# Kernel optimization log

Measured on AMD Instinct MI355X. Metric: run time of the kernel, lower is better.

The kernel has to match this reference:

```python
import jax, jax.numpy as jnp
import numpy as np

E, CAP, D, F = 8, 4096, 1024, 4096  # experts, capacity/expert, d_model, d_ff


def setup_inputs() -> dict:
    key = jax.random.key(0)
    k0, k1, k2 = jax.random.split(key, 3)
    inputs = jax.random.normal(k0, (1, E * CAP, D), dtype=jnp.float32)
    # per-expert FFN params (stacked over expert axis)
    W1 = jax.random.normal(k1, (E, D, F), dtype=jnp.float32) * (1.0 / np.sqrt(D))
    b1 = jnp.zeros((E, F), dtype=jnp.float32)
    W2 = jax.random.normal(k2, (E, F, D), dtype=jnp.float32) * (1.0 / np.sqrt(F))
    b2 = jnp.zeros((E, D), dtype=jnp.float32)
    return {"inputs": inputs, "W1": W1, "b1": b1, "W2": W2, "b2": b2}


def reference(inputs, W1, b1, W2, b2):
    # inputs: [B, E*C, D]. chunk(dim=1) over E experts == reshape to [B, E, C, D].
    B, T, D_ = inputs.shape
    x = inputs.reshape(B, E, T // E, D_)  # [B, E, C, D]
    # grouped GEMM form of the per-expert loop: each expert applies its own FFN
    h = jax.nn.gelu(jnp.einsum('becd,edf->becf', x, W1) + b1[None, :, None, :])
    y = jnp.einsum('becf,efd->becd', h, W2) + b2[None, :, None, :]
    # cat over dim=1 == reshape back
    return y.reshape(B, T, D_)
```

## Files before the change

### kernel.cpp

```cpp
#include <hip/hip_runtime.h>
#include <stdint.h>

#define E_ 8
#define C_ 4096
#define D_ 1024
#define F_ 4096

typedef __attribute__((ext_vector_type(8))) short bf16x8;
typedef __attribute__((ext_vector_type(4))) float f32x4;
typedef __attribute__((ext_vector_type(8))) unsigned short u16x8;
typedef __attribute__((ext_vector_type(4))) unsigned short u16x4;

__device__ __forceinline__ unsigned short f2bf(float x) {
  union { float f; uint32_t u; } v; v.f = x;
  uint32_t r = v.u + 0x7FFFu + ((v.u >> 16) & 1u);
  return (unsigned short)(r >> 16);
}

__device__ __forceinline__ float gelu_f(float x) {
  float x3 = x * x * x;
  float u = 0.7978845608028654f * __builtin_fmaf(0.044715f, x3, x);
  float t = __expf(2.0f * u);
  float th = 1.0f - 2.0f / (t + 1.0f);
  return 0.5f * x * (1.0f + th);
}

__global__ void convert_bf16_kernel(const float* __restrict__ in,
                                    unsigned short* __restrict__ out, size_t n) {
  size_t i = ((size_t)blockIdx.x * blockDim.x + threadIdx.x) * 8;
  size_t stride = (size_t)gridDim.x * blockDim.x * 8;
  for (; i < n; i += stride) {
    float4 a = *(const float4*)(in + i);
    float4 b = *(const float4*)(in + i + 4);
    u16x8 o;
    o[0] = f2bf(a.x); o[1] = f2bf(a.y); o[2] = f2bf(a.z); o[3] = f2bf(a.w);
    o[4] = f2bf(b.x); o[5] = f2bf(b.y); o[6] = f2bf(b.z); o[7] = f2bf(b.w);
    *(u16x8*)(out + i) = o;
  }
}

__global__ void transpose_bf16_kernel(const float* __restrict__ in,
                                      unsigned short* __restrict__ out,
                                      int K, int N) {
  const int ge = blockIdx.z;
  const float* src = in + (size_t)ge * K * N;
  unsigned short* dst = out + (size_t)ge * K * N;
  __shared__ float tile[32][33];
  int t = threadIdx.x;
  int tx = t & 31, ty = t >> 5;
  int k0 = blockIdx.x * 32, n0 = blockIdx.y * 32;
#pragma unroll
  for (int p = 0; p < 4; ++p)
    tile[ty + p * 8][tx] = src[(size_t)(k0 + ty + p * 8) * N + n0 + tx];
  __syncthreads();
#pragma unroll
  for (int p = 0; p < 4; ++p)
    dst[(size_t)(n0 + ty + p * 8) * K + k0 + tx] = f2bf(tile[tx][ty + p * 8]);
}

typedef const __attribute__((address_space(1))) uint32_t* gas1_ptr;
typedef __attribute__((address_space(3))) uint32_t* las3_ptr;

__device__ __forceinline__ void async16(const void* g, void* l) {
  __builtin_amdgcn_global_load_lds((gas1_ptr)(uintptr_t)g, (las3_ptr)(uintptr_t)l,
                                   16, 0, 0);
}


#define SYNC_PRE() do { \
    __builtin_amdgcn_sched_barrier(0); \
    __builtin_amdgcn_s_barrier(); \
    asm volatile("s_waitcnt lgkmcnt(0)" ::: "memory"); \
    __builtin_amdgcn_sched_barrier(0); \
    __builtin_amdgcn_s_setprio(1); \
  } while (0)

#define SYNC_POST() do { \
    __builtin_amdgcn_s_setprio(0); \
    __builtin_amdgcn_sched_barrier(0); \
    __builtin_amdgcn_s_barrier(); \
    __builtin_amdgcn_sched_barrier(0); \
  } while (0)

#define SYNC_POST_VM() do { \
    __builtin_amdgcn_s_setprio(0); \
    __builtin_amdgcn_sched_barrier(0); \
    asm volatile("s_waitcnt vmcnt(6)" ::: "memory"); \
    __builtin_amdgcn_s_barrier(); \
    __builtin_amdgcn_sched_barrier(0); \
  } while (0)

template <int MODE>
__global__ __launch_bounds__(512, 2) void gemm256_kernel(
    const unsigned short* __restrict__ A,
    const unsigned short* __restrict__ B,
    const float* __restrict__ bias,
    void* __restrict__ Cout,
    int K, int N, int numM, int numN,
    size_t aStride, size_t bStride, size_t cStride, int biasStride) {
  __shared__ char lds[131072];
  char* ldsp = (char*)lds;

  const int NT = K >> 6;
  const int NITER = NT >> 1;

  int lin = blockIdx.x;
  int nwg = gridDim.x;
  int qq = nwg >> 3, rr8 = nwg & 7;
  int xcd = lin & 7, idx = lin >> 3;
  int wg = (xcd < rr8 ? xcd * (qq + 1) : rr8 * (qq + 1) + (xcd - rr8) * qq) + idx;
  int per = numM * numN;
  int e = wg / per;
  int rem = wg - e * per;
  int tm = rem % numM, tn = rem / numM;

  A += (size_t)e * aStride;
  B += (size_t)e * bStride;
  bias += (size_t)e * biasStride;

  const int rowTile = tm << 8;
  const int colTile = tn << 8;

  const int tid = threadIdx.x;
  const int lane = tid & 63;
  const int w = tid >> 6;
  const int wm = w & 1, wn = w >> 1;
  const int l15 = lane & 15, q = lane >> 4;

  const size_t ldB = (size_t)K * 2;

  const int rlo = tid >> 3, kc = tid & 7;
  const int swzsrc = ((kc ^ (rlo & 7)) << 4);
  const char* aS0 = (const char*)A + (size_t)(rowTile + rlo) * ldB + swzsrc;
  const char* aS1 = (const char*)A + (size_t)(rowTile + rlo + 128) * ldB + swzsrc;
  const int bcol = (rlo & 31) + ((rlo >> 5) << 6);
  const char* bS0 = (const char*)B + (size_t)(colTile + bcol) * ldB + swzsrc;
  const char* bS1 = (const char*)B + (size_t)(colTile + bcol + 128) * ldB + swzsrc;
  const size_t a64 = (size_t)64 * ldB;
  const size_t b32 = (size_t)32 * ldB;
  const int aD0 = rlo * 128 + kc * 16;
  const int aD1 = aD0 + 16384;
  const int bD0 = 32768 + bcol * 128 + kc * 16;
  const int bD1 = bD0 + 16384;

#define STAGE_A(bb, Ah, kt) do { \
    size_t kb = (size_t)(kt) * 128; \
    int dbase = (bb) * 65536 + (Ah) * 8192; \
    async16(aS0 + (Ah) * a64 + kb, ldsp + dbase + aD0); \
    async16(aS1 + (Ah) * a64 + kb, ldsp + dbase + aD1); \
  } while (0)

#define STAGE_B(bb, Bh, kt) do { \
    size_t kb = (size_t)(kt) * 128; \
    int dbase = (bb) * 65536 + (Bh) * 4096; \
    async16(bS0 + (Bh) * b32 + kb, ldsp + dbase + bD0); \
    async16(bS1 + (Bh) * b32 + kb, ldsp + dbase + bD1); \
  } while (0)

  const int k0 = (q * 16) ^ ((l15 & 7) << 4);
  const int aRdBase = wm * 16384 + l15 * 128;
  const int bRdBase = 32768 + wn * 8192 + l15 * 128;

  bf16x8 aR[4][2], bR0[2][2], bR1[2][2];
  f32x4 acc[8][4];
#pragma unroll
  for (int m = 0; m < 8; ++m)
#pragma unroll
    for (int n = 0; n < 4; ++n) acc[m][n] = {0.f, 0.f, 0.f, 0.f};

#define READ_A(bb, mh) do { \
    _Pragma("unroll") for (int m4 = 0; m4 < 4; ++m4) \
    _Pragma("unroll") for (int ks = 0; ks < 2; ++ks) \
      aR[m4][ks] = *(const bf16x8*)(ldsp + (bb) * 65536 + aRdBase + \
                                    ((mh) * 4 + m4) * 2048 + (k0 ^ (ks << 6))); \
  } while (0)

#define READ_B(dst, bb, nh) do { \
    _Pragma("unroll") for (int n2 = 0; n2 < 2; ++n2) \
    _Pragma("unroll") for (int ks = 0; ks < 2; ++ks) \
      dst[n2][ks] = *(const bf16x8*)(ldsp + (bb) * 65536 + bRdBase + \
                                     ((nh) * 2 + n2) * 2048 + (k0 ^ (ks << 6))); \
  } while (0)

#define MFMA_QUAD(mh, nh, BR) do { \
    _Pragma("unroll") for (int m4 = 0; m4 < 4; ++m4) \
    _Pragma("unroll") for (int n2 = 0; n2 < 2; ++n2) \
    _Pragma("unroll") for (int ks = 0; ks < 2; ++ks) \
      acc[(mh) * 4 + m4][(nh) * 2 + n2] = \
          __builtin_amdgcn_mfma_f32_16x16x32_bf16( \
              BR[n2][ks], aR[m4][ks], acc[(mh) * 4 + m4][(nh) * 2 + n2], 0, 0, 0); \
  } while (0)

  STAGE_A(0, 0, 0); STAGE_B(0, 0, 0); STAGE_A(0, 1, 0); STAGE_B(0, 1, 0);
  STAGE_A(1, 0, 1); STAGE_B(1, 0, 1); STAGE_A(1, 1, 1);
  asm volatile("s_waitcnt vmcnt(6)" ::: "memory");
  __builtin_amdgcn_sched_barrier(0);
  __builtin_amdgcn_s_barrier();
  __builtin_amdgcn_sched_barrier(0);

  for (int j = 0; j < NITER; ++j) {
    int t1 = 2 * j + 1;
    int t2 = 2 * j + 2; if (t2 > NT - 1) t2 = NT - 1;
    int t3 = 2 * j + 3; if (t3 > NT - 1) t3 = NT - 1;

    READ_A(0, 0); READ_B(bR0, 0, 0);
    STAGE_B(1, 1, t1);
    SYNC_PRE(); MFMA_QUAD(0, 0, bR0); SYNC_POST();
    READ_B(bR1, 0, 1);
    STAGE_A(0, 0, t2);
    SYNC_PRE(); MFMA_QUAD(0, 1, bR1); SYNC_POST();
    READ_A(0, 1);
    STAGE_B(0, 0, t2);
    SYNC_PRE(); MFMA_QUAD(1, 1, bR1); SYNC_POST();
    STAGE_A(0, 1, t2);
    SYNC_PRE(); MFMA_QUAD(1, 0, bR0); SYNC_POST_VM();
    READ_A(1, 0); READ_B(bR0, 1, 0);
    STAGE_B(0, 1, t2);
    SYNC_PRE(); MFMA_QUAD(0, 0, bR0); SYNC_POST();
    READ_B(bR1, 1, 1);
    STAGE_A(1, 0, t3);
    SYNC_PRE(); MFMA_QUAD(0, 1, bR1); SYNC_POST();
    READ_A(1, 1);
    STAGE_B(1, 0, t3);
    SYNC_PRE(); MFMA_QUAD(1, 1, bR1); SYNC_POST();
    STAGE_A(1, 1, t3);
    SYNC_PRE(); MFMA_QUAD(1, 0, bR0); SYNC_POST_VM();
  }
  asm volatile("s_waitcnt vmcnt(0)" ::: "memory");

#pragma unroll
  for (int mf = 0; mf < 8; ++mf) {
    int row = rowTile + wm * 128 + mf * 16 + l15;
#pragma unroll
    for (int nf = 0; nf < 4; ++nf) {
      int col = colTile + wn * 64 + nf * 16 + q * 4;
      float4 bv = *(const float4*)(bias + col);
      f32x4 v = acc[mf][nf];
      if constexpr (MODE == 1) {
        u16x4 o;
        o[0] = f2bf(gelu_f(v[0] + bv.x));
        o[1] = f2bf(gelu_f(v[1] + bv.y));
        o[2] = f2bf(gelu_f(v[2] + bv.z));
        o[3] = f2bf(gelu_f(v[3] + bv.w));
        *(u16x4*)((unsigned short*)Cout + (size_t)e * cStride +
                  (size_t)row * N + col) = o;
      } else {
        float4 o;
        o.x = v[0] + bv.x; o.y = v[1] + bv.y;
        o.z = v[2] + bv.z; o.w = v[3] + bv.w;
        *(float4*)((float*)Cout + (size_t)e * cStride + (size_t)row * N + col) = o;
      }
    }
  }
}

extern "C" void kernel_launch(void* const* d_in, const int* in_sizes, int n_in,
                              void* d_out, int out_size, void* d_ws, size_t ws_size,
                              hipStream_t stream) {
  const float* X = (const float*)d_in[0];
  const float* W1 = (const float*)d_in[1];
  const float* b1 = (const float*)d_in[2];
  const float* W2 = (const float*)d_in[3];
  const float* b2 = (const float*)d_in[4];
  float* Y = (float*)d_out;

  const size_t szX = (size_t)C_ * D_ * 2;
  const size_t szW1 = (size_t)F_ * D_ * 2;
  const size_t szW2 = (size_t)D_ * F_ * 2;
  const size_t szH = (size_t)C_ * F_ * 2;
  const size_t fixed = szX + szW1 + szW2;

  int g = 0;
  {
    const int cands[4] = {8, 4, 2, 1};
    for (int i = 0; i < 4; ++i)
      if ((fixed + szH) * (size_t)cands[i] <= ws_size) { g = cands[i]; break; }
  }
  int RC = C_;
  if (g == 0) {
    g = 1;
    size_t avail = ws_size > fixed ? ws_size - fixed : 0;
    RC = (int)(avail / ((size_t)F_ * 2));
    RC = (RC / 256) * 256;
    if (RC < 256) RC = 256;
    if (RC > C_) RC = C_;
  }

  unsigned short* XB = (unsigned short*)d_ws;
  unsigned short* W1T = XB + (size_t)g * C_ * D_;
  unsigned short* W2T = W1T + (size_t)g * F_ * D_;
  unsigned short* H = W2T + (size_t)g * D_ * F_;

  const int numN1 = F_ / 256;
  const int numN2 = D_ / 256;

  for (int e0 = 0; e0 < E_; e0 += g) {
    {
      size_t n = (size_t)g * C_ * D_;
      size_t nb = (n / 8 + 255) / 256;
      if (nb > 2048) nb = 2048;
      convert_bf16_kernel<<<dim3((unsigned)nb), 256, 0, stream>>>(
          X + (size_t)e0 * C_ * D_, XB, n);
    }
    transpose_bf16_kernel<<<dim3(D_ / 32, F_ / 32, g), 256, 0, stream>>>(
        W1 + (size_t)e0 * D_ * F_, W1T, D_, F_);
    transpose_bf16_kernel<<<dim3(F_ / 32, D_ / 32, g), 256, 0, stream>>>(
        W2 + (size_t)e0 * F_ * D_, W2T, F_, D_);

    for (int r0 = 0; r0 < C_; r0 += RC) {
      int numM = RC / 256;
      gemm256_kernel<1><<<dim3((unsigned)(numM * numN1 * g)), 512, 0, stream>>>(
          XB + (size_t)r0 * D_, W1T, b1 + (size_t)e0 * F_, (void*)H,
          D_, F_, numM, numN1,
          (size_t)C_ * D_, (size_t)F_ * D_, (size_t)RC * F_, F_);
      gemm256_kernel<0><<<dim3((unsigned)(numM * numN2 * g)), 512, 0, stream>>>(
          H, W2T, b2 + (size_t)e0 * D_,
          (void*)(Y + (size_t)e0 * C_ * D_ + (size_t)r0 * D_),
          F_, D_, numM, numN2,
          (size_t)RC * F_, (size_t)D_ * F_, (size_t)C_ * D_, D_);
    }
  }
}
```

Before: 725.2 us.

## Double-buffer LDS fragment registers and relax waitcnts in grouped GEMM main loop

Reworks the 256x256 bf16 MFMA main loop so A and B fragments are double-buffered in registers (even/odd sets), with next-phase LDS reads issued before the current MFMA quad. Waits are relaxed from full lgkmcnt(0) to partial vmcnt/lgkmcnt counts, letting LDS reads and global-to-LDS loads overlap with the MFMAs. Address arithmetic is simplified into precomputed int offsets, and the order of the prologue and in-loop staging is changed. This raises register pressure and relies on hand-tuned wait counts, which risk races if any count is wrong.

New measurement: 849.4 us. +17.1%, slower.

```diff
diff --git a/kernel.cpp b/kernel.cpp
--- a/kernel.cpp
+++ b/kernel.cpp
@@ -67,10 +67,10 @@
 }
 
 
-#define SYNC_PRE() do { \
+#define SYNC_PRE(VM, LG) do { \
     __builtin_amdgcn_sched_barrier(0); \
     __builtin_amdgcn_s_barrier(); \
-    asm volatile("s_waitcnt lgkmcnt(0)" ::: "memory"); \
+    asm volatile("s_waitcnt vmcnt(" #VM ") lgkmcnt(" #LG ")" ::: "memory"); \
     __builtin_amdgcn_sched_barrier(0); \
     __builtin_amdgcn_s_setprio(1); \
   } while (0)
@@ -78,14 +78,6 @@
 #define SYNC_POST() do { \
     __builtin_amdgcn_s_setprio(0); \
     __builtin_amdgcn_sched_barrier(0); \
-    __builtin_amdgcn_s_barrier(); \
-    __builtin_amdgcn_sched_barrier(0); \
-  } while (0)
-
-#define SYNC_POST_VM() do { \
-    __builtin_amdgcn_s_setprio(0); \
-    __builtin_amdgcn_sched_barrier(0); \
-    asm volatile("s_waitcnt vmcnt(6)" ::: "memory"); \
     __builtin_amdgcn_s_barrier(); \
     __builtin_amdgcn_sched_barrier(0); \
   } while (0)
@@ -131,102 +123,110 @@
 
   const int rlo = tid >> 3, kc = tid & 7;
   const int swzsrc = ((kc ^ (rlo & 7)) << 4);
-  const char* aS0 = (const char*)A + (size_t)(rowTile + rlo) * ldB + swzsrc;
-  const char* aS1 = (const char*)A + (size_t)(rowTile + rlo + 128) * ldB + swzsrc;
+  const int vA = (int)(rlo * (int)ldB) + swzsrc;
   const int bcol = (rlo & 31) + ((rlo >> 5) << 6);
-  const char* bS0 = (const char*)B + (size_t)(colTile + bcol) * ldB + swzsrc;
-  const char* bS1 = (const char*)B + (size_t)(colTile + bcol + 128) * ldB + swzsrc;
-  const size_t a64 = (size_t)64 * ldB;
-  const size_t b32 = (size_t)32 * ldB;
-  const int aD0 = rlo * 128 + kc * 16;
-  const int aD1 = aD0 + 16384;
-  const int bD0 = 32768 + bcol * 128 + kc * 16;
-  const int bD1 = bD0 + 16384;
+  const int vB = (int)(bcol * (int)ldB) + swzsrc;
+  const int dA = tid * 16;
+  const int dB = 32768 + (rlo & 31) * 128 + (rlo >> 5) * 8192 + kc * 16;
+  const char* Ag = (const char*)A + (size_t)rowTile * ldB;
+  const char* Bg = (const char*)B + (size_t)colTile * ldB;
+  const size_t r128 = (size_t)128 * ldB;
 
 #define STAGE_A(bb, Ah, kt) do { \
-    size_t kb = (size_t)(kt) * 128; \
-    int dbase = (bb) * 65536 + (Ah) * 8192; \
-    async16(aS0 + (Ah) * a64 + kb, ldsp + dbase + aD0); \
-    async16(aS1 + (Ah) * a64 + kb, ldsp + dbase + aD1); \
+    size_t u = (size_t)((Ah) * 64) * ldB + (size_t)(kt) * 128; \
+    async16(Ag + u + vA, ldsp + (bb) * 65536 + (Ah) * 8192 + dA); \
+    async16(Ag + u + r128 + vA, \
+            ldsp + (bb) * 65536 + (Ah) * 8192 + 16384 + dA); \
   } while (0)
 
 #define STAGE_B(bb, Bh, kt) do { \
-    size_t kb = (size_t)(kt) * 128; \
-    int dbase = (bb) * 65536 + (Bh) * 4096; \
-    async16(bS0 + (Bh) * b32 + kb, ldsp + dbase + bD0); \
-    async16(bS1 + (Bh) * b32 + kb, ldsp + dbase + bD1); \
+    size_t u = (size_t)((Bh) * 32) * ldB + (size_t)(kt) * 128; \
+    async16(Bg + u + vB, ldsp + (bb) * 65536 + (Bh) * 4096 + dB); \
+    async16(Bg + u + r128 + vB, \
+            ldsp + (bb) * 65536 + (Bh) * 4096 + 16384 + dB); \
   } while (0)
 
   const int k0 = (q * 16) ^ ((l15 & 7) << 4);
-  const int aRdBase = wm * 16384 + l15 * 128;
-  const int bRdBase = 32768 + wn * 8192 + l15 * 128;
-
-  bf16x8 aR[4][2], bR0[2][2], bR1[2][2];
+  const int iA00 = wm * 16384 + l15 * 128 + k0;
+  const int iA01 = iA00 ^ 64;
+  const int iA10 = iA00 + 65536;
+  const int iA11 = iA01 + 65536;
+  const int iB00 = 32768 + wn * 8192 + l15 * 128 + k0;
+  const int iB01 = iB00 ^ 64;
+  const int iB10 = iB00 + 65536;
+  const int iB11 = iB01 + 65536;
+
+  bf16x8 aE[4][2], aO[4][2], bZ[2][2], bY[2][2];
   f32x4 acc[8][4];
 #pragma unroll
   for (int m = 0; m < 8; ++m)
 #pragma unroll
     for (int n = 0; n < 4; ++n) acc[m][n] = {0.f, 0.f, 0.f, 0.f};
 
-#define READ_A(bb, mh) do { \
-    _Pragma("unroll") for (int m4 = 0; m4 < 4; ++m4) \
-    _Pragma("unroll") for (int ks = 0; ks < 2; ++ks) \
-      aR[m4][ks] = *(const bf16x8*)(ldsp + (bb) * 65536 + aRdBase + \
-                                    ((mh) * 4 + m4) * 2048 + (k0 ^ (ks << 6))); \
-  } while (0)
-
-#define READ_B(dst, bb, nh) do { \
-    _Pragma("unroll") for (int n2 = 0; n2 < 2; ++n2) \
-    _Pragma("unroll") for (int ks = 0; ks < 2; ++ks) \
-      dst[n2][ks] = *(const bf16x8*)(ldsp + (bb) * 65536 + bRdBase + \
-                                     ((nh) * 2 + n2) * 2048 + (k0 ^ (ks << 6))); \
-  } while (0)
-
-#define MFMA_QUAD(mh, nh, BR) do { \
+#define READ_A(dst, b0, b1, mh) do { \
+    _Pragma("unroll") for (int m4 = 0; m4 < 4; ++m4) { \
+      dst[m4][0] = *(const bf16x8*)(ldsp + (b0) + (mh) * 8192 + m4 * 2048); \
+      dst[m4][1] = *(const bf16x8*)(ldsp + (b1) + (mh) * 8192 + m4 * 2048); \
+    } \
+  } while (0)
+
+#define READ_B(dst, b0, b1, nh) do { \
+    _Pragma("unroll") for (int n2 = 0; n2 < 2; ++n2) { \
+      dst[n2][0] = *(const bf16x8*)(ldsp + (b0) + (nh) * 4096 + n2 * 2048); \
+      dst[n2][1] = *(const bf16x8*)(ldsp + (b1) + (nh) * 4096 + n2 * 2048); \
+    } \
+  } while (0)
+
+#define MFMA_Q(mh, nh, AF, BF) do { \
     _Pragma("unroll") for (int m4 = 0; m4 < 4; ++m4) \
     _Pragma("unroll") for (int n2 = 0; n2 < 2; ++n2) \
     _Pragma("unroll") for (int ks = 0; ks < 2; ++ks) \
       acc[(mh) * 4 + m4][(nh) * 2 + n2] = \
           __builtin_amdgcn_mfma_f32_16x16x32_bf16( \
-              BR[n2][ks], aR[m4][ks], acc[(mh) * 4 + m4][(nh) * 2 + n2], 0, 0, 0); \
-  } while (0)
-
-  STAGE_A(0, 0, 0); STAGE_B(0, 0, 0); STAGE_A(0, 1, 0); STAGE_B(0, 1, 0);
-  STAGE_A(1, 0, 1); STAGE_B(1, 0, 1); STAGE_A(1, 1, 1);
+              BF[n2][ks], AF[m4][ks], acc[(mh) * 4 + m4][(nh) * 2 + n2], 0, 0, 0); \
+  } while (0)
+
+  STAGE_A(0, 0, 0); STAGE_B(0, 0, 0); STAGE_B(0, 1, 0); STAGE_A(0, 1, 0);
+  STAGE_A(1, 0, 1); STAGE_B(1, 0, 1); STAGE_B(1, 1, 1);
   asm volatile("s_waitcnt vmcnt(6)" ::: "memory");
   __builtin_amdgcn_sched_barrier(0);
   __builtin_amdgcn_s_barrier();
   __builtin_amdgcn_sched_barrier(0);
+  READ_A(aE, iA00, iA01, 0);
+  READ_B(bZ, iB00, iB01, 0);
 
   for (int j = 0; j < NITER; ++j) {
     int t1 = 2 * j + 1;
     int t2 = 2 * j + 2; if (t2 > NT - 1) t2 = NT - 1;
     int t3 = 2 * j + 3; if (t3 > NT - 1) t3 = NT - 1;
 
-    READ_A(0, 0); READ_B(bR0, 0, 0);
-    STAGE_B(1, 1, t1);
-    SYNC_PRE(); MFMA_QUAD(0, 0, bR0); SYNC_POST();
-    READ_B(bR1, 0, 1);
+    READ_B(bY, iB00, iB01, 1);
+    STAGE_A(1, 1, t1);
+    SYNC_PRE(8, 4); MFMA_Q(0, 0, aE, bZ); SYNC_POST();
+    READ_A(aO, iA00, iA01, 1);
     STAGE_A(0, 0, t2);
-    SYNC_PRE(); MFMA_QUAD(0, 1, bR1); SYNC_POST();
-    READ_A(0, 1);
+    SYNC_PRE(8, 8); MFMA_Q(0, 1, aE, bY); SYNC_POST();
     STAGE_B(0, 0, t2);
-    SYNC_PRE(); MFMA_QUAD(1, 1, bR1); SYNC_POST();
+    SYNC_PRE(8, 0); MFMA_Q(1, 0, aO, bZ); SYNC_POST();
+    READ_A(aE, iA10, iA11, 0);
+    READ_B(bZ, iB10, iB11, 0);
+    STAGE_B(0, 1, t2);
+    SYNC_PRE(8, 12); MFMA_Q(1, 1, aO, bY); SYNC_POST();
+    READ_B(bY, iB10, iB11, 1);
     STAGE_A(0, 1, t2);
-    SYNC_PRE(); MFMA_QUAD(1, 0, bR0); SYNC_POST_VM();
-    READ_A(1, 0); READ_B(bR0, 1, 0);
-    STAGE_B(0, 1, t2);
-    SYNC_PRE(); MFMA_QUAD(0, 0, bR0); SYNC_POST();
-    READ_B(bR1, 1, 1);
+    SYNC_PRE(8, 4); MFMA_Q(0, 0, aE, bZ); SYNC_POST();
+    READ_A(aO, iA10, iA11, 1);
     STAGE_A(1, 0, t3);
-    SYNC_PRE(); MFMA_QUAD(0, 1, bR1); SYNC_POST();
-    READ_A(1, 1);
+    SYNC_PRE(8, 8); MFMA_Q(0, 1, aE, bY); SYNC_POST();
     STAGE_B(1, 0, t3);
-    SYNC_PRE(); MFMA_QUAD(1, 1, bR1); SYNC_POST();
-    STAGE_A(1, 1, t3);
-    SYNC_PRE(); MFMA_QUAD(1, 0, bR0); SYNC_POST_VM();
-  }
-  asm volatile("s_waitcnt vmcnt(0)" ::: "memory");
+    SYNC_PRE(8, 0); MFMA_Q(1, 0, aO, bZ); SYNC_POST();
+    READ_A(aE, iA00, iA01, 0);
+    READ_B(bZ, iB00, iB01, 0);
+    STAGE_B(1, 1, t3);
+    SYNC_PRE(8, 12); MFMA_Q(1, 1, aO, bY); SYNC_POST();
+  }
+  asm volatile("s_waitcnt vmcnt(0) lgkmcnt(0)" ::: "memory");
+  __builtin_amdgcn_sched_barrier(0);
 
 #pragma unroll
   for (int mf = 0; mf < 8; ++mf) {
```

## Pre-pack operands into tile-contiguous blocks and restructure GEMM pipeline

Applied to the files above, without the earlier changes.

Replaces the bf16 convert and transpose kernels with pack kernels that write X, W1 and W2 as contiguous 256x64 tile blocks. The GEMM then streams each K-tile with eight linear 16-byte async loads per thread instead of swizzled strided rows. The first GEMM writes H directly in that packed layout, so the second GEMM consumes it the same way. The main loop is rebuilt with full-tile double buffering, a vmcnt(0) wait per tile, and register double-buffered fragments. The fp32 output epilogue is staged through LDS for coalesced row stores. The aim is to cut address arithmetic and uncoalesced loads, at the cost of more barriers in the epilogue and a possibly less deep prefetch.

New measurement: 860.6 us. 1.19x slower.

```diff
diff --git a/kernel.cpp b/kernel.cpp
--- a/kernel.cpp
+++ b/kernel.cpp
@@ -25,37 +25,65 @@
   return 0.5f * x * (1.0f + th);
 }
 
-__global__ void convert_bf16_kernel(const float* __restrict__ in,
-                                    unsigned short* __restrict__ out, size_t n) {
-  size_t i = ((size_t)blockIdx.x * blockDim.x + threadIdx.x) * 8;
-  size_t stride = (size_t)gridDim.x * blockDim.x * 8;
-  for (; i < n; i += stride) {
-    float4 a = *(const float4*)(in + i);
-    float4 b = *(const float4*)(in + i + 4);
-    u16x8 o;
-    o[0] = f2bf(a.x); o[1] = f2bf(a.y); o[2] = f2bf(a.z); o[3] = f2bf(a.w);
-    o[4] = f2bf(b.x); o[5] = f2bf(b.y); o[6] = f2bf(b.z); o[7] = f2bf(b.w);
-    *(u16x8*)(out + i) = o;
-  }
-}
-
-__global__ void transpose_bf16_kernel(const float* __restrict__ in,
-                                      unsigned short* __restrict__ out,
-                                      int K, int N) {
-  const int ge = blockIdx.z;
-  const float* src = in + (size_t)ge * K * N;
-  unsigned short* dst = out + (size_t)ge * K * N;
-  __shared__ float tile[32][33];
-  int t = threadIdx.x;
-  int tx = t & 31, ty = t >> 5;
-  int k0 = blockIdx.x * 32, n0 = blockIdx.y * 32;
-#pragma unroll
-  for (int p = 0; p < 4; ++p)
-    tile[ty + p * 8][tx] = src[(size_t)(k0 + ty + p * 8) * N + n0 + tx];
+
+__global__ __launch_bounds__(256) void pack_rm_kernel(
+    const float* __restrict__ in, unsigned short* __restrict__ out,
+    int R, int K) {
+  const int p = blockIdx.x, t = blockIdx.y, ge = blockIdx.z;
+  const float* src = in + (size_t)ge * R * K + (size_t)(p * 256) * K + t * 64;
+  unsigned short* dst =
+      out + ((size_t)(ge * (R >> 8) + p) * (K >> 6) + t) * 16384;
+  __shared__ unsigned short sm[256 * 72];
+  const int tid = threadIdx.x;
+  const int rb = tid >> 4, k4 = (tid & 15) * 4;
+#pragma unroll
+  for (int i = 0; i < 16; ++i) {
+    int r = rb + i * 16;
+    float4 v = *(const float4*)(src + (size_t)r * K + k4);
+    u16x4 o;
+    o[0] = f2bf(v.x); o[1] = f2bf(v.y); o[2] = f2bf(v.z); o[3] = f2bf(v.w);
+    *(u16x4*)&sm[r * 72 + k4] = o;
+  }
   __syncthreads();
 #pragma unroll
-  for (int p = 0; p < 4; ++p)
-    dst[(size_t)(n0 + ty + p * 8) * K + k0 + tx] = f2bf(tile[tx][ty + p * 8]);
+  for (int w = 0; w < 8; ++w) {
+    int o = tid * 8 + w * 2048;
+    int h = o >> 13, c = (o >> 10) & 7, r7 = (o >> 3) & 127;
+    int row = h * 128 + r7;
+    u16x8 v = *(const u16x8*)&sm[row * 72 + c * 8];
+    *(u16x8*)(dst + o) = v;
+  }
+}
+
+__global__ __launch_bounds__(256) void pack_tr_kernel(
+    const float* __restrict__ in, unsigned short* __restrict__ out,
+    int K, int N) {
+  const int pn = blockIdx.x, tk = blockIdx.y, ge = blockIdx.z;
+  const float* src = in + (size_t)ge * K * N + (size_t)(tk * 64) * N + pn * 256;
+  unsigned short* dst =
+      out + ((size_t)(ge * (N >> 8) + pn) * (K >> 6) + tk) * 16384;
+  __shared__ unsigned short sm[64 * 260];
+  const int tid = threadIdx.x;
+  const int kb = tid >> 6, n4 = (tid & 63) * 4;
+#pragma unroll
+  for (int i = 0; i < 16; ++i) {
+    int kk = kb + i * 4;
+    float4 v = *(const float4*)(src + (size_t)kk * N + n4);
+    u16x4 o;
+    o[0] = f2bf(v.x); o[1] = f2bf(v.y); o[2] = f2bf(v.z); o[3] = f2bf(v.w);
+    *(u16x4*)&sm[kk * 260 + n4] = o;
+  }
+  __syncthreads();
+#pragma unroll
+  for (int w = 0; w < 8; ++w) {
+    int o = tid * 8 + w * 2048;
+    int h = o >> 13, c = (o >> 10) & 7, r7 = (o >> 3) & 127;
+    int n = h * 128 + r7;
+    u16x8 v;
+#pragma unroll
+    for (int e = 0; e < 8; ++e) v[e] = sm[(c * 8 + e) * 260 + n];
+    *(u16x8*)(dst + o) = v;
+  }
 }
 
 typedef const __attribute__((address_space(1))) uint32_t* gas1_ptr;
@@ -67,7 +95,7 @@
 }
 
 
-#define SYNC_PRE() do { \
+#define PRE_LG() do { \
     __builtin_amdgcn_sched_barrier(0); \
     __builtin_amdgcn_s_barrier(); \
     asm volatile("s_waitcnt lgkmcnt(0)" ::: "memory"); \
@@ -75,17 +103,18 @@
     __builtin_amdgcn_s_setprio(1); \
   } while (0)
 
-#define SYNC_POST() do { \
+#define PRE_VM() do { \
+    __builtin_amdgcn_sched_barrier(0); \
+    asm volatile("s_waitcnt vmcnt(0)" ::: "memory"); \
+    __builtin_amdgcn_s_barrier(); \
+    asm volatile("s_waitcnt lgkmcnt(0)" ::: "memory"); \
+    __builtin_amdgcn_sched_barrier(0); \
+    __builtin_amdgcn_s_setprio(1); \
+  } while (0)
+
+#define POST() do { \
     __builtin_amdgcn_s_setprio(0); \
     __builtin_amdgcn_sched_barrier(0); \
-    __builtin_amdgcn_s_barrier(); \
-    __builtin_amdgcn_sched_barrier(0); \
-  } while (0)
-
-#define SYNC_POST_VM() do { \
-    __builtin_amdgcn_s_setprio(0); \
-    __builtin_amdgcn_sched_barrier(0); \
-    asm volatile("s_waitcnt vmcnt(6)" ::: "memory"); \
     __builtin_amdgcn_s_barrier(); \
     __builtin_amdgcn_sched_barrier(0); \
   } while (0)
@@ -102,7 +131,6 @@
   char* ldsp = (char*)lds;
 
   const int NT = K >> 6;
-  const int NITER = NT >> 1;
 
   int lin = blockIdx.x;
   int nwg = gridDim.x;
@@ -114,10 +142,6 @@
   int rem = wg - e * per;
   int tm = rem % numM, tn = rem / numM;
 
-  A += (size_t)e * aStride;
-  B += (size_t)e * bStride;
-  bias += (size_t)e * biasStride;
-
   const int rowTile = tm << 8;
   const int colTile = tn << 8;
 
@@ -127,129 +151,152 @@
   const int wm = w & 1, wn = w >> 1;
   const int l15 = lane & 15, q = lane >> 4;
 
-  const size_t ldB = (size_t)K * 2;
-
-  const int rlo = tid >> 3, kc = tid & 7;
-  const int swzsrc = ((kc ^ (rlo & 7)) << 4);
-  const char* aS0 = (const char*)A + (size_t)(rowTile + rlo) * ldB + swzsrc;
-  const char* aS1 = (const char*)A + (size_t)(rowTile + rlo + 128) * ldB + swzsrc;
-  const int bcol = (rlo & 31) + ((rlo >> 5) << 6);
-  const char* bS0 = (const char*)B + (size_t)(colTile + bcol) * ldB + swzsrc;
-  const char* bS1 = (const char*)B + (size_t)(colTile + bcol + 128) * ldB + swzsrc;
-  const size_t a64 = (size_t)64 * ldB;
-  const size_t b32 = (size_t)32 * ldB;
-  const int aD0 = rlo * 128 + kc * 16;
-  const int aD1 = aD0 + 16384;
-  const int bD0 = 32768 + bcol * 128 + kc * 16;
-  const int bD1 = bD0 + 16384;
-
-#define STAGE_A(bb, Ah, kt) do { \
-    size_t kb = (size_t)(kt) * 128; \
-    int dbase = (bb) * 65536 + (Ah) * 8192; \
-    async16(aS0 + (Ah) * a64 + kb, ldsp + dbase + aD0); \
-    async16(aS1 + (Ah) * a64 + kb, ldsp + dbase + aD1); \
-  } while (0)
-
-#define STAGE_B(bb, Bh, kt) do { \
-    size_t kb = (size_t)(kt) * 128; \
-    int dbase = (bb) * 65536 + (Bh) * 4096; \
-    async16(bS0 + (Bh) * b32 + kb, ldsp + dbase + bD0); \
-    async16(bS1 + (Bh) * b32 + kb, ldsp + dbase + bD1); \
-  } while (0)
-
-  const int k0 = (q * 16) ^ ((l15 & 7) << 4);
-  const int aRdBase = wm * 16384 + l15 * 128;
-  const int bRdBase = 32768 + wn * 8192 + l15 * 128;
-
-  bf16x8 aR[4][2], bR0[2][2], bR1[2][2];
+  const char* Ag = (const char*)(A + (size_t)e * aStride) +
+                   (size_t)tm * NT * 32768 + tid * 16;
+  const char* Bg = (const char*)(B + (size_t)e * bStride) +
+                   (size_t)tn * NT * 32768 + tid * 16;
+  char* ldT = ldsp + tid * 16;
+
+#define STAGE_ALL(bb, kt) do { \
+    const char* as_ = Ag + (size_t)(kt) * 32768; \
+    const char* bs_ = Bg + (size_t)(kt) * 32768; \
+    char* ld_ = ldT + (bb) * 65536; \
+    async16(as_, ld_);                      async16(as_ + 8192, ld_ + 8192); \
+    async16(as_ + 16384, ld_ + 16384);      async16(as_ + 24576, ld_ + 24576); \
+    async16(bs_, ld_ + 32768);              async16(bs_ + 8192, ld_ + 40960); \
+    async16(bs_ + 16384, ld_ + 49152);      async16(bs_ + 24576, ld_ + 57344); \
+  } while (0)
+
+  const int aRd = wm * 16384 + q * 2048 + l15 * 16;
+  const int bRd = 32768 + (wn >> 1) * 16384 + q * 2048 +
+                  ((wn & 1) * 64 + l15) * 16;
+
+  bf16x8 aE[4][2], aO[4][2], bZ[2][2], bY[2][2];
   f32x4 acc[8][4];
 #pragma unroll
   for (int m = 0; m < 8; ++m)
 #pragma unroll
     for (int n = 0; n < 4; ++n) acc[m][n] = {0.f, 0.f, 0.f, 0.f};
 
-#define READ_A(bb, mh) do { \
+#define READ_A(dst, bb, mh) do { \
     _Pragma("unroll") for (int m4 = 0; m4 < 4; ++m4) \
     _Pragma("unroll") for (int ks = 0; ks < 2; ++ks) \
-      aR[m4][ks] = *(const bf16x8*)(ldsp + (bb) * 65536 + aRdBase + \
-                                    ((mh) * 4 + m4) * 2048 + (k0 ^ (ks << 6))); \
+      dst[m4][ks] = *(const bf16x8*)(ldsp + (bb) * 65536 + aRd + ks * 8192 + \
+                                     (mh) * 1024 + m4 * 256); \
   } while (0)
 
 #define READ_B(dst, bb, nh) do { \
     _Pragma("unroll") for (int n2 = 0; n2 < 2; ++n2) \
     _Pragma("unroll") for (int ks = 0; ks < 2; ++ks) \
-      dst[n2][ks] = *(const bf16x8*)(ldsp + (bb) * 65536 + bRdBase + \
-                                     ((nh) * 2 + n2) * 2048 + (k0 ^ (ks << 6))); \
-  } while (0)
-
-#define MFMA_QUAD(mh, nh, BR) do { \
+      dst[n2][ks] = *(const bf16x8*)(ldsp + (bb) * 65536 + bRd + ks * 8192 + \
+                                     (nh) * 512 + n2 * 256); \
+  } while (0)
+
+#define MFMA_Q(mh, nh, AF, BF) do { \
     _Pragma("unroll") for (int m4 = 0; m4 < 4; ++m4) \
     _Pragma("unroll") for (int n2 = 0; n2 < 2; ++n2) \
     _Pragma("unroll") for (int ks = 0; ks < 2; ++ks) \
       acc[(mh) * 4 + m4][(nh) * 2 + n2] = \
           __builtin_amdgcn_mfma_f32_16x16x32_bf16( \
-              BR[n2][ks], aR[m4][ks], acc[(mh) * 4 + m4][(nh) * 2 + n2], 0, 0, 0); \
-  } while (0)
-
-  STAGE_A(0, 0, 0); STAGE_B(0, 0, 0); STAGE_A(0, 1, 0); STAGE_B(0, 1, 0);
-  STAGE_A(1, 0, 1); STAGE_B(1, 0, 1); STAGE_A(1, 1, 1);
-  asm volatile("s_waitcnt vmcnt(6)" ::: "memory");
+              BF[n2][ks], AF[m4][ks], acc[(mh) * 4 + m4][(nh) * 2 + n2], 0, 0, 0); \
+  } while (0)
+
+#define TILE_BODY(bb, nb, tnext) do { \
+     \
+    PRE_LG(); \
+    STAGE_ALL(nb, tnext); \
+    READ_B(bY, bb, 1); \
+    MFMA_Q(0, 0, aE, bZ); \
+    POST(); \
+     \
+    PRE_LG(); \
+    READ_A(aO, bb, 1); \
+    MFMA_Q(0, 1, aE, bY); \
+    POST(); \
+     \
+    PRE_VM(); \
+    READ_A(aE, nb, 0); \
+    MFMA_Q(1, 0, aO, bZ); \
+    POST(); \
+     \
+    PRE_LG(); \
+    READ_B(bZ, nb, 0); \
+    MFMA_Q(1, 1, aO, bY); \
+    POST(); \
+  } while (0)
+
+  STAGE_ALL(0, 0);
+  asm volatile("s_waitcnt vmcnt(0)" ::: "memory");
   __builtin_amdgcn_sched_barrier(0);
   __builtin_amdgcn_s_barrier();
   __builtin_amdgcn_sched_barrier(0);
-
-  for (int j = 0; j < NITER; ++j) {
+  READ_A(aE, 0, 0);
+  READ_B(bZ, 0, 0);
+
+  const int NP = NT >> 1;
+  for (int j = 0; j < NP; ++j) {
     int t1 = 2 * j + 1;
     int t2 = 2 * j + 2; if (t2 > NT - 1) t2 = NT - 1;
-    int t3 = 2 * j + 3; if (t3 > NT - 1) t3 = NT - 1;
-
-    READ_A(0, 0); READ_B(bR0, 0, 0);
-    STAGE_B(1, 1, t1);
-    SYNC_PRE(); MFMA_QUAD(0, 0, bR0); SYNC_POST();
-    READ_B(bR1, 0, 1);
-    STAGE_A(0, 0, t2);
-    SYNC_PRE(); MFMA_QUAD(0, 1, bR1); SYNC_POST();
-    READ_A(0, 1);
-    STAGE_B(0, 0, t2);
-    SYNC_PRE(); MFMA_QUAD(1, 1, bR1); SYNC_POST();
-    STAGE_A(0, 1, t2);
-    SYNC_PRE(); MFMA_QUAD(1, 0, bR0); SYNC_POST_VM();
-    READ_A(1, 0); READ_B(bR0, 1, 0);
-    STAGE_B(0, 1, t2);
-    SYNC_PRE(); MFMA_QUAD(0, 0, bR0); SYNC_POST();
-    READ_B(bR1, 1, 1);
-    STAGE_A(1, 0, t3);
-    SYNC_PRE(); MFMA_QUAD(0, 1, bR1); SYNC_POST();
-    READ_A(1, 1);
-    STAGE_B(1, 0, t3);
-    SYNC_PRE(); MFMA_QUAD(1, 1, bR1); SYNC_POST();
-    STAGE_A(1, 1, t3);
-    SYNC_PRE(); MFMA_QUAD(1, 0, bR0); SYNC_POST_VM();
-  }
-  asm volatile("s_waitcnt vmcnt(0)" ::: "memory");
-
-#pragma unroll
-  for (int mf = 0; mf < 8; ++mf) {
-    int row = rowTile + wm * 128 + mf * 16 + l15;
+    TILE_BODY(0, 1, t1);
+    TILE_BODY(1, 0, t2);
+  }
+  asm volatile("s_waitcnt vmcnt(0) lgkmcnt(0)" ::: "memory");
+  __builtin_amdgcn_sched_barrier(0);
+
+  if constexpr (MODE == 1) {
+    unsigned short* Hb = (unsigned short*)Cout + (size_t)e * cStride;
+    unsigned short* Hw = Hb +
+        ((size_t)(tm * (N >> 6) + tn * 4 + wn) * 2 + wm) * 8192 +
+        (q >> 1) * 1024 + l15 * 8 + (q & 1) * 4;
 #pragma unroll
     for (int nf = 0; nf < 4; ++nf) {
       int col = colTile + wn * 64 + nf * 16 + q * 4;
-      float4 bv = *(const float4*)(bias + col);
-      f32x4 v = acc[mf][nf];
-      if constexpr (MODE == 1) {
+      float4 bv = *(const float4*)(bias + e * biasStride + col);
+#pragma unroll
+      for (int mf = 0; mf < 8; ++mf) {
+        f32x4 v = acc[mf][nf];
         u16x4 o;
         o[0] = f2bf(gelu_f(v[0] + bv.x));
         o[1] = f2bf(gelu_f(v[1] + bv.y));
         o[2] = f2bf(gelu_f(v[2] + bv.z));
         o[3] = f2bf(gelu_f(v[3] + bv.w));
-        *(u16x4*)((unsigned short*)Cout + (size_t)e * cStride +
-                  (size_t)row * N + col) = o;
-      } else {
-        float4 o;
-        o.x = v[0] + bv.x; o.y = v[1] + bv.y;
-        o.z = v[2] + bv.z; o.w = v[3] + bv.w;
-        *(float4*)((float*)Cout + (size_t)e * cStride + (size_t)row * N + col) = o;
+        *(u16x4*)(Hw + nf * 2048 + mf * 128) = o;
       }
+    }
+  } else {
+    __syncthreads();
+    float* smf = (float*)ldsp;
+    float* Yb = (float*)Cout + (size_t)e * cStride;
+    const int srow = wm * 16 + l15;
+    float4 bv[4];
+#pragma unroll
+    for (int nf = 0; nf < 4; ++nf)
+      bv[nf] = *(const float4*)(bias + e * biasStride + colTile + wn * 64 +
+                                nf * 16 + q * 4);
+#pragma unroll
+    for (int mf = 0; mf < 8; ++mf) {
+#pragma unroll
+      for (int nf = 0; nf < 4; ++nf) {
+        f32x4 v = acc[mf][nf];
+        f32x4 o = {v[0] + bv[nf].x, v[1] + bv[nf].y,
+                   v[2] + bv[nf].z, v[3] + bv[nf].w};
+        *(f32x4*)&smf[srow * 260 + wn * 64 + nf * 16 + q * 4] = o;
+      }
+      __syncthreads();
+      {
+        int r32 = tid >> 4, seg = tid & 15;
+        int row = rowTile + (r32 >> 4) * 128 + mf * 16 + (r32 & 15);
+        float* yr = Yb + (size_t)row * N + colTile + seg * 16;
+        float4 v0 = *(float4*)&smf[r32 * 260 + seg * 16 + 0];
+        float4 v1 = *(float4*)&smf[r32 * 260 + seg * 16 + 4];
+        float4 v2 = *(float4*)&smf[r32 * 260 + seg * 16 + 8];
+        float4 v3 = *(float4*)&smf[r32 * 260 + seg * 16 + 12];
+        *(float4*)(yr + 0) = v0;
+        *(float4*)(yr + 4) = v1;
+        *(float4*)(yr + 8) = v2;
+        *(float4*)(yr + 12) = v3;
+      }
+      __syncthreads();
     }
   }
 }
@@ -286,35 +333,31 @@
     if (RC > C_) RC = C_;
   }
 
-  unsigned short* XB = (unsigned short*)d_ws;
-  unsigned short* W1T = XB + (size_t)g * C_ * D_;
-  unsigned short* W2T = W1T + (size_t)g * F_ * D_;
-  unsigned short* H = W2T + (size_t)g * D_ * F_;
+  unsigned short* XP = (unsigned short*)d_ws;
+  unsigned short* W1P = XP + (size_t)g * C_ * D_;
+  unsigned short* W2P = W1P + (size_t)g * F_ * D_;
+  unsigned short* HP = W2P + (size_t)g * D_ * F_;
 
   const int numN1 = F_ / 256;
   const int numN2 = D_ / 256;
+  const int NT1 = D_ / 64;
 
   for (int e0 = 0; e0 < E_; e0 += g) {
-    {
-      size_t n = (size_t)g * C_ * D_;
-      size_t nb = (n / 8 + 255) / 256;
-      if (nb > 2048) nb = 2048;
-      convert_bf16_kernel<<<dim3((unsigned)nb), 256, 0, stream>>>(
-          X + (size_t)e0 * C_ * D_, XB, n);
-    }
-    transpose_bf16_kernel<<<dim3(D_ / 32, F_ / 32, g), 256, 0, stream>>>(
-        W1 + (size_t)e0 * D_ * F_, W1T, D_, F_);
-    transpose_bf16_kernel<<<dim3(F_ / 32, D_ / 32, g), 256, 0, stream>>>(
-        W2 + (size_t)e0 * F_ * D_, W2T, F_, D_);
+    pack_rm_kernel<<<dim3(C_ / 256, D_ / 64, g), 256, 0, stream>>>(
+        X + (size_t)e0 * C_ * D_, XP, C_, D_);
+    pack_tr_kernel<<<dim3(F_ / 256, D_ / 64, g), 256, 0, stream>>>(
+        W1 + (size_t)e0 * D_ * F_, W1P, D_, F_);
+    pack_tr_kernel<<<dim3(D_ / 256, F_ / 64, g), 256, 0, stream>>>(
+        W2 + (size_t)e0 * F_ * D_, W2P, F_, D_);
 
     for (int r0 = 0; r0 < C_; r0 += RC) {
       int numM = RC / 256;
       gemm256_kernel<1><<<dim3((unsigned)(numM * numN1 * g)), 512, 0, stream>>>(
-          XB + (size_t)r0 * D_, W1T, b1 + (size_t)e0 * F_, (void*)H,
-          D_, F_, numM, numN1,
+          XP + (size_t)(r0 >> 8) * NT1 * 16384, W1P, b1 + (size_t)e0 * F_,
+          (void*)HP, D_, F_, numM, numN1,
           (size_t)C_ * D_, (size_t)F_ * D_, (size_t)RC * F_, F_);
       gemm256_kernel<0><<<dim3((unsigned)(numM * numN2 * g)), 512, 0, stream>>>(
-          H, W2T, b2 + (size_t)e0 * D_,
+          HP, W2P, b2 + (size_t)e0 * D_,
           (void*)(Y + (size_t)e0 * C_ * D_ + (size_t)r0 * D_),
           F_, D_, numM, numN2,
           (size_t)RC * F_, (size_t)D_ * F_, (size_t)C_ * D_, D_);
```
